# Optimization experiments

Hardware: AMD Instinct MI355X
Metric: run time of the kernel (lower is better)

The kernel has to match this reference:

```python
import jax, jax.numpy as jnp
import numpy as np

B, T, C, H = 32, 576, 1024, 16
D = C // H  # head_dim = 64

def setup_inputs() -> dict:
    key = jax.random.key(0)
    ks = jax.random.split(key, 5)
    s = 1.0 / np.sqrt(C)
    return {
        "emb_img": jax.random.normal(ks[0], (B, T, C), dtype=jnp.float32),
        "w_qkv": jax.random.normal(ks[1], (C, 3 * C), dtype=jnp.float32) * s,
        "b_qkv": jnp.zeros((3 * C,), dtype=jnp.float32),
        "w_proj": jax.random.normal(ks[2], (C, C), dtype=jnp.float32) * s,
        "b_proj": jnp.zeros((C,), dtype=jnp.float32),
    }

def reference(emb_img, w_qkv, b_qkv, w_proj, b_proj):
    # fused QKV projection
    qkv = emb_img @ w_qkv + b_qkv                       # [B,T,3C]
    q, k, v = jnp.split(qkv, 3, axis=-1)                # each [B,T,C]
    def heads(x):
        return x.reshape(B, T, H, D).transpose(0, 2, 1, 3)  # [B,H,T,D]
    q, k, v = heads(q), heads(k), heads(v)
    # note: original scales by 1/head_dim (not 1/sqrt(head_dim))
    scores = jnp.einsum("bhqd,bhkd->bhqk", q, k) * (1.0 / D)
    causal = jnp.tril(jnp.ones((T, T), dtype=bool))
    scores = jnp.where(causal[None, None], scores, -jnp.inf)
    att = jax.nn.softmax(scores, axis=-1)               # [B,H,T,T]
    y = jnp.einsum("bhqk,bhkd->bhqd", att, v)           # [B,H,T,D]
    y = y.transpose(0, 2, 1, 3).reshape(B, T, C)
    return y @ w_proj + b_proj
```

## Files before the change

kernel.cpp:

```cpp
#include <hip/hip_runtime.h>
#include <stdint.h>

namespace {

constexpr int kB = 32, kT = 576, kC = 1024, kH = 16, kD = 64;
constexpr int kM = kB * kT;
constexpr int kNqkv = 3 * kC;
constexpr float kQScale = 1.4426950408889634f / 64.0f;

typedef uint16_t u16;
typedef __attribute__((ext_vector_type(4))) float f32x4;
typedef __attribute__((ext_vector_type(8))) short short8;
typedef __attribute__((ext_vector_type(8))) __bf16 bf16x8;
typedef __attribute__((ext_vector_type(4))) uint16_t u16x4;

#define VMCNT(n) asm volatile("s_waitcnt vmcnt(" #n ")" ::: "memory")

__device__ __forceinline__ float fexp2(float x) {
  return __builtin_amdgcn_exp2f(x);
}

__device__ __forceinline__ f32x4 mfma_bf16(short8 a, short8 b, f32x4 c) {
  return __builtin_amdgcn_mfma_f32_16x16x32_bf16(
      __builtin_bit_cast(bf16x8, a), __builtin_bit_cast(bf16x8, b), c, 0, 0, 0);
}

__device__ __forceinline__ u16 to_bf16(float x) {
  uint32_t u = __float_as_uint(x);
  u += 0x7fffu + ((u >> 16) & 1u);
  return (u16)(u >> 16);
}

__device__ __forceinline__ void gload_lds16(const void* g, void* l) {
  __builtin_amdgcn_global_load_lds(
      (const __attribute__((address_space(1))) uint32_t*)(uintptr_t)g,
      (__attribute__((address_space(3))) uint32_t*)(uintptr_t)l,
      16, 0, 0);
}

__device__ __forceinline__ void bar() {
  asm volatile("" ::: "memory");
  __builtin_amdgcn_s_barrier();
  asm volatile("" ::: "memory");
}

__global__ __launch_bounds__(256) void cvt_bf16_kernel(
    const float* __restrict__ in, u16* __restrict__ out, int n4) {
  const int i = blockIdx.x * 256 + threadIdx.x;
  if (i >= n4) return;
  const f32x4 v = ((const f32x4*)in)[i];
  u16x4 o;
#pragma unroll
  for (int j = 0; j < 4; ++j) o[j] = to_bf16(v[j]);
  ((u16x4*)out)[i] = o;
}

__global__ void tconv_kernel(const float* __restrict__ in, u16* __restrict__ out,
                             int K, int N) {
  __shared__ u16 tile[32][33];
  const int nb = blockIdx.x * 32;
  const int kb = blockIdx.y * 32;
  const int tx = threadIdx.x;
  const int ty = threadIdx.y;
#pragma unroll
  for (int i = 0; i < 32; i += 8)
    tile[ty + i][tx] = to_bf16(in[(size_t)(kb + ty + i) * N + nb + tx]);
  __syncthreads();
#pragma unroll
  for (int i = 0; i < 32; i += 8)
    out[(size_t)(nb + ty + i) * K + kb + tx] = tile[tx][ty + i];
}

__global__ __launch_bounds__(512, 4) void gemm_qkv(
    const u16* __restrict__ A, const u16* __restrict__ Bt,
    const float* __restrict__ bias,
    u16* __restrict__ outQ, u16* __restrict__ outK, u16* __restrict__ outVT) {
  constexpr int Kc = 1024;
  constexpr int NT = Kc / 32;
  __shared__ char lds[3][24576];

  const int tid = threadIdx.x;
  const int wave = tid >> 6;
  const int lane = tid & 63;
  const int lo = lane & 15;
  const int hi = lane >> 4;
  const int wr = wave >> 1;
  const int wc = wave & 1;

  const int lin = blockIdx.x + blockIdx.y * 24;
  const int l2 = (lin & 7) * 216 + (lin >> 3);
  const int n0 = (l2 % 24) * 128;
  const int m0 = (l2 / 24) * 256;

  const u16* srcA[2];
#pragma unroll
  for (int c = 0; c < 2; ++c) {
    const int off = c * 8192 + tid * 16;
    const int p = off >> 7;
    const int col = (off & 127) ^ ((p & 7) << 4);
    const int Ar = (col < 64) ? p : p + 128;
    const int k_ = (col & 63) >> 1;
    srcA[c] = A + (size_t)(m0 + Ar) * Kc + k_;
  }
  const u16* srcB1;
  {
    const int off = tid * 16;
    const int p = off >> 7;
    const int col = (off & 127) ^ ((p & 7) << 4);
    const int Br = (col < 64) ? p : p + 64;
    const int k_ = (col & 63) >> 1;
    srcB1 = Bt + (size_t)(n0 + Br) * Kc + k_;
  }

  auto stage = [&](int slot, int t) {
    char* base = &lds[slot][0];
    gload_lds16(srcA[0] + t * 32, base + tid * 16);
    gload_lds16(srcA[1] + t * 32, base + 8192 + tid * 16);
    gload_lds16(srcB1 + t * 32, base + 16384 + tid * 16);
  };

  f32x4 acc[4][4] = {};

  auto compute = [&](int slot) {
    const char* base = &lds[slot][0];
    const char* baseB = base + 16384;
    const int swz = (lo & 7) << 4;
    short8 af[4], bf[4];
#pragma unroll
    for (int i = 0; i < 4; ++i) {
      const int row = wr * 64 + i * 16 + lo;
      const int prow = row & 127;
      const int half = row >> 7;
      af[i] = *(const short8*)(base + prow * 128 + ((half * 64 + hi * 16) ^ swz));
    }
#pragma unroll
    for (int j = 0; j < 4; ++j) {
      const int row = wc * 64 + j * 16 + lo;
      const int prow = row & 63;
      const int half = row >> 6;
      bf[j] = *(const short8*)(baseB + prow * 128 + ((half * 64 + hi * 16) ^ swz));
    }
    __builtin_amdgcn_s_setprio(1);
#pragma unroll
    for (int i = 0; i < 4; ++i)
#pragma unroll
      for (int j = 0; j < 4; ++j)
        acc[i][j] = mfma_bf16(af[i], bf[j], acc[i][j]);
    __builtin_amdgcn_s_setprio(0);
  };

  stage(0, 0);
  stage(1, 1);
  for (int t = 0; t < NT; ++t) {
    if (t + 1 < NT) { VMCNT(3); } else { VMCNT(0); }
    bar();
    compute(t % 3);
    if (t + 2 < NT) stage((t + 2) % 3, t + 2);
  }
  bar();

  if (n0 >= 2048) {
    u16* wlds = (u16*)&lds[0][0] + wave * (32 * 66);
    uint32_t* wlds32 = (uint32_t*)wlds;
#pragma unroll
    for (int jp = 0; jp < 2; ++jp) {
#pragma unroll
      for (int jj = 0; jj < 2; ++jj) {
        const int j = jp * 2 + jj;
        const int n = n0 + wc * 64 + j * 16 + lo;
        const float bv = bias[n];
        const int dl = jj * 16 + lo;
#pragma unroll
        for (int i = 0; i < 4; ++i)
#pragma unroll
          for (int rp = 0; rp < 2; ++rp) {
            const u16 w0 = to_bf16(acc[i][j][rp * 2] + bv);
            const u16 w1 = to_bf16(acc[i][j][rp * 2 + 1] + bv);
            wlds32[dl * 33 + i * 8 + hi * 2 + rp] =
                (uint32_t)w0 | ((uint32_t)w1 << 16);
          }
      }
#pragma unroll
      for (int p = 0; p < 8; ++p) {
        const int dl32 = p * 4 + hi;
        const int n = n0 + wc * 64 + jp * 32 + dl32;
        const int c = n & 1023;
        const int hh = c >> 6;
        const int d = c & 63;
        const int m = m0 + wr * 64 + lo * 4;
        const int bb = m / kT;
        const int t = m - bb * kT;
        const u16x4 v = *(const u16x4*)&wlds[dl32 * 66 + lo * 4];
        *(u16x4*)&outVT[((size_t)(bb * kH + hh) * kD + d) * kT + t] = v;
      }
    }
  } else {
#pragma unroll
    for (int j = 0; j < 4; ++j) {
      const int n = n0 + wc * 64 + j * 16 + lo;
      const float bv = bias[n];
      const int which = n >> 10;
      const int c = n & 1023;
      const int hh = c >> 6;
      const int d = c & 63;
#pragma unroll
      for (int i = 0; i < 4; ++i) {
        const int mrow = m0 + wr * 64 + i * 16 + hi * 4;
#pragma unroll
        for (int r = 0; r < 4; ++r) {
          const int m = mrow + r;
          const int bb = m / kT;
          const int t = m - bb * kT;
          const float v = acc[i][j][r] + bv;
          if (which == 0)
            outQ[((size_t)(bb * kH + hh) * kT + t) * kD + d] = to_bf16(v * kQScale);
          else
            outK[((size_t)(bb * kH + hh) * kT + t) * kD + d] = to_bf16(v);
        }
      }
    }
  }
}

__global__ __launch_bounds__(512, 4) void gemm_proj(
    const u16* __restrict__ A, const u16* __restrict__ Bt,
    const float* __restrict__ bias, float* __restrict__ outF) {
  constexpr int Kc = 1024;
  constexpr int NT = Kc / 32;
  __shared__ char lds[3][24576];

  const int tid = threadIdx.x;
  const int wave = tid >> 6;
  const int lane = tid & 63;
  const int lo = lane & 15;
  const int hi = lane >> 4;
  const int wr = wave >> 1;
  const int wc = wave & 1;

  const int lin = blockIdx.x + blockIdx.y * 8;
  const int l2 = (lin & 7) * 72 + (lin >> 3);
  const int n0 = (l2 % 8) * 128;
  const int m0 = (l2 / 8) * 256;

  const u16* srcA[2];
#pragma unroll
  for (int c = 0; c < 2; ++c) {
    const int off = c * 8192 + tid * 16;
    const int p = off >> 7;
    const int col = (off & 127) ^ ((p & 7) << 4);
    const int Ar = (col < 64) ? p : p + 128;
    const int k_ = (col & 63) >> 1;
    srcA[c] = A + (size_t)(m0 + Ar) * Kc + k_;
  }
  const u16* srcB1;
  {
    const int off = tid * 16;
    const int p = off >> 7;
    const int col = (off & 127) ^ ((p & 7) << 4);
    const int Br = (col < 64) ? p : p + 64;
    const int k_ = (col & 63) >> 1;
    srcB1 = Bt + (size_t)(n0 + Br) * Kc + k_;
  }

  auto stage = [&](int slot, int t) {
    char* base = &lds[slot][0];
    gload_lds16(srcA[0] + t * 32, base + tid * 16);
    gload_lds16(srcA[1] + t * 32, base + 8192 + tid * 16);
    gload_lds16(srcB1 + t * 32, base + 16384 + tid * 16);
  };

  f32x4 acc[4][4] = {};

  auto compute = [&](int slot) {
    const char* base = &lds[slot][0];
    const char* baseB = base + 16384;
    const int swz = (lo & 7) << 4;
    short8 af[4], bf[4];
#pragma unroll
    for (int i = 0; i < 4; ++i) {
      const int row = wr * 64 + i * 16 + lo;
      const int prow = row & 127;
      const int half = row >> 7;
      af[i] = *(const short8*)(base + prow * 128 + ((half * 64 + hi * 16) ^ swz));
    }
#pragma unroll
    for (int j = 0; j < 4; ++j) {
      const int row = wc * 64 + j * 16 + lo;
      const int prow = row & 63;
      const int half = row >> 6;
      bf[j] = *(const short8*)(baseB + prow * 128 + ((half * 64 + hi * 16) ^ swz));
    }
    __builtin_amdgcn_s_setprio(1);
#pragma unroll
    for (int i = 0; i < 4; ++i)
#pragma unroll
      for (int j = 0; j < 4; ++j)
        acc[i][j] = mfma_bf16(af[i], bf[j], acc[i][j]);
    __builtin_amdgcn_s_setprio(0);
  };

  stage(0, 0);
  stage(1, 1);
  for (int t = 0; t < NT; ++t) {
    if (t + 1 < NT) { VMCNT(3); } else { VMCNT(0); }
    bar();
    compute(t % 3);
    if (t + 2 < NT) stage((t + 2) % 3, t + 2);
  }

#pragma unroll
  for (int j = 0; j < 4; ++j) {
    const int n = n0 + wc * 64 + j * 16 + lo;
    const float bv = bias[n];
#pragma unroll
    for (int i = 0; i < 4; ++i) {
      const int mrow = m0 + wr * 64 + i * 16 + hi * 4;
#pragma unroll
      for (int r = 0; r < 4; ++r)
        outF[(size_t)(mrow + r) * kC + n] = acc[i][j][r] + bv;
    }
  }
}

__global__ __launch_bounds__(256) void attn_kernel(
    const u16* __restrict__ Q, const u16* __restrict__ K,
    const u16* __restrict__ VT, u16* __restrict__ Y) {
  __shared__ u16 P[4][32][72];

  const int idx = blockIdx.x;
  const int qi = 4 - (idx >> 9);
  const int bh = idx & 511;
  const int wave = threadIdx.x >> 6;
  const int lane = threadIdx.x & 63;
  const int lo = lane & 15;
  const int hi = lane >> 4;
  const int q0 = qi * 128 + wave * 32;
  if (q0 >= kT) return;

  const u16* Qb = Q + (size_t)bh * kT * kD;
  const u16* Kb = K + (size_t)bh * kT * kD;
  const u16* Vb = VT + (size_t)bh * kD * kT;

  short8 qf[2][2];
#pragma unroll
  for (int h = 0; h < 2; ++h) {
    const u16* qp = Qb + (q0 + h * 16 + lo) * kD + hi * 8;
    qf[h][0] = *(const short8*)qp;
    qf[h][1] = *(const short8*)(qp + 32);
  }

  f32x4 acc[2][4] = {};
  float mrun[2] = {-3e38f, -3e38f};
  float lsum[2] = {0.f, 0.f};

  short8 kf[4][2];
#pragma unroll
  for (int kc = 0; kc < 4; ++kc) {
    const u16* kp = Kb + (kc * 16 + lo) * kD + hi * 8;
    kf[kc][0] = *(const short8*)kp;
    kf[kc][1] = *(const short8*)(kp + 32);
  }

  const int nfull = q0 >> 6;
  const bool tail4 = ((q0 >> 5) & 1) != 0;

  auto do_tile = [&](int kv, int kclim, bool masked, bool have_next,
                     bool next_wide) {
    f32x4 s[2][4];
#pragma unroll
    for (int kc = 0; kc < 4; ++kc) {
      if (kc < kclim) {
#pragma unroll
        for (int h = 0; h < 2; ++h) {
          f32x4 z = {0.f, 0.f, 0.f, 0.f};
          z = mfma_bf16(kf[kc][0], qf[h][0], z);
          z = mfma_bf16(kf[kc][1], qf[h][1], z);
          s[h][kc] = z;
        }
      }
    }
    short8 vf[4][2];
#pragma unroll
    for (int nt = 0; nt < 4; ++nt) {
      const u16* vp = Vb + (nt * 16 + lo) * kT + kv + hi * 8;
      vf[nt][0] = *(const short8*)vp;
      if (kclim == 4) vf[nt][1] = *(const short8*)(vp + 32);
    }
    if (have_next) {
#pragma unroll
      for (int kc = 0; kc < 2; ++kc) {
        const u16* kp = Kb + (kv + 64 + kc * 16 + lo) * kD + hi * 8;
        kf[kc][0] = *(const short8*)kp;
        kf[kc][1] = *(const short8*)(kp + 32);
      }
      if (next_wide) {
#pragma unroll
        for (int kc = 2; kc < 4; ++kc) {
          const u16* kp = Kb + (kv + 64 + kc * 16 + lo) * kD + hi * 8;
          kf[kc][0] = *(const short8*)kp;
          kf[kc][1] = *(const short8*)(kp + 32);
        }
      }
    }
    if (masked) {
#pragma unroll
      for (int h = 0; h < 2; ++h) {
        const int q = q0 + h * 16 + lo;
#pragma unroll
        for (int kc = 0; kc < 4; ++kc)
          if (kc < kclim) {
#pragma unroll
            for (int r = 0; r < 4; ++r)
              if (kv + kc * 16 + hi * 4 + r > q) s[h][kc][r] = -3e38f;
          }
      }
    }
#pragma unroll
    for (int h = 0; h < 2; ++h) {
      float pm;
      {
        float m01 = fmaxf(fmaxf(s[h][0][0], s[h][0][1]),
                          fmaxf(s[h][0][2], s[h][0][3]));
        float m23 = fmaxf(fmaxf(s[h][1][0], s[h][1][1]),
                          fmaxf(s[h][1][2], s[h][1][3]));
        pm = fmaxf(m01, m23);
        if (kclim == 4) {
          float m45 = fmaxf(fmaxf(s[h][2][0], s[h][2][1]),
                            fmaxf(s[h][2][2], s[h][2][3]));
          float m67 = fmaxf(fmaxf(s[h][3][0], s[h][3][1]),
                            fmaxf(s[h][3][2], s[h][3][3]));
          pm = fmaxf(pm, fmaxf(m45, m67));
        }
      }
      pm = fmaxf(pm, __shfl_xor(pm, 16));
      pm = fmaxf(pm, __shfl_xor(pm, 32));
      const float mnew = fmaxf(mrun[h], pm);
      const float corr = fexp2(mrun[h] - mnew);
      mrun[h] = mnew;
      float psum = 0.f;
#pragma unroll
      for (int kc = 0; kc < 4; ++kc)
        if (kc < kclim) {
          u16x4 pk;
#pragma unroll
          for (int r = 0; r < 4; ++r) {
            const float pv = fexp2(s[h][kc][r] - mnew);
            psum += pv;
            pk[r] = to_bf16(pv);
          }
          *(u16x4*)&P[wave][h * 16 + lo][kc * 16 + hi * 4] = pk;
        }
      lsum[h] = lsum[h] * corr + psum;
#pragma unroll
      for (int nt = 0; nt < 4; ++nt)
#pragma unroll
        for (int r = 0; r < 4; ++r) acc[h][nt][r] *= corr;
      const short8 pf0 = *(const short8*)&P[wave][h * 16 + lo][hi * 8];
      short8 pf1;
      if (kclim == 4) pf1 = *(const short8*)&P[wave][h * 16 + lo][32 + hi * 8];
#pragma unroll
      for (int nt = 0; nt < 4; ++nt) {
        acc[h][nt] = mfma_bf16(pf0, vf[nt][0], acc[h][nt]);
        if (kclim == 4) acc[h][nt] = mfma_bf16(pf1, vf[nt][1], acc[h][nt]);
      }
    }
  };

  for (int it = 0; it < nfull; ++it)
    do_tile(it * 64, 4, false, true, (it + 1 < nfull) || tail4);
  if (tail4) do_tile(nfull * 64, 4, true, false, false);
  else       do_tile(nfull * 64, 2, true, false, false);

#pragma unroll
  for (int h = 0; h < 2; ++h) {
    lsum[h] += __shfl_xor(lsum[h], 16);
    lsum[h] += __shfl_xor(lsum[h], 32);
  }
  const int b = bh >> 4, hh = bh & 15;
#pragma unroll
  for (int h = 0; h < 2; ++h)
#pragma unroll
    for (int r = 0; r < 4; ++r) {
      const float linv = 1.0f / __shfl(lsum[h], hi * 4 + r);
      const int t = q0 + h * 16 + hi * 4 + r;
      const size_t base = ((size_t)(b * kT + t) * kH + hh) * kD;
#pragma unroll
      for (int nt = 0; nt < 4; ++nt)
        Y[base + nt * 16 + lo] = to_bf16(acc[h][nt][r] * linv);
    }
}

}

extern "C" void kernel_launch(void* const* d_in, const int* in_sizes, int n_in,
                              void* d_out, int out_size, void* d_ws, size_t ws_size,
                              hipStream_t stream) {
  (void)in_sizes; (void)n_in; (void)out_size; (void)ws_size;
  const float* emb   = (const float*)d_in[0];
  const float* wqkv  = (const float*)d_in[1];
  const float* bqkv  = (const float*)d_in[2];
  const float* wproj = (const float*)d_in[3];
  const float* bproj = (const float*)d_in[4];
  float* out = (float*)d_out;

  char* p = (char*)d_ws;
  u16* embb   = (u16*)p; p += (size_t)kM * kC * 2;
  u16* wqkvt  = (u16*)p; p += (size_t)kNqkv * kC * 2;
  u16* wprojt = (u16*)p; p += (size_t)kC * kC * 2;
  u16* Qh     = (u16*)p; p += (size_t)kM * kC * 2;
  u16* Kh     = (u16*)p; p += (size_t)kM * kC * 2;
  u16* VTh    = (u16*)p; p += (size_t)kM * kC * 2;
  u16* Yh     = (u16*)p; p += (size_t)kM * kC * 2;

  const int n4 = kM * kC / 4;
  cvt_bf16_kernel<<<dim3((n4 + 255) / 256), 256, 0, stream>>>(emb, embb, n4);
  tconv_kernel<<<dim3(kNqkv / 32, kC / 32), dim3(32, 8), 0, stream>>>(wqkv, wqkvt, kC, kNqkv);
  tconv_kernel<<<dim3(kC / 32, kC / 32), dim3(32, 8), 0, stream>>>(wproj, wprojt, kC, kC);
  gemm_qkv<<<dim3(kNqkv / 128, kM / 256), 512, 0, stream>>>(
      embb, wqkvt, bqkv, Qh, Kh, VTh);
  attn_kernel<<<dim3(5 * kB * kH), 256, 0, stream>>>(Qh, Kh, VTh, Yh);
  gemm_proj<<<dim3(kC / 128, kM / 256), 512, 0, stream>>>(
      Yh, wprojt, bproj, out);
}
```

Before: 320.2 us.

## Shrink proj GEMM tile to 128x128 with double-buffered LDS pipeline

The output-projection GEMM moves from 256x128 tiles with 512 threads and a triple-buffered LDS pipeline to 128x128 tiles with 256 threads and double buffering. This doubles the grid to 1152 blocks and cuts LDS per block, with the aim of better occupancy and CU load balance. The cost is lower operand reuse per tile and an extra barrier per k-step, since the next stage is now issued before compute. The L2-friendly block remap is adjusted to the new grid shape.

```diff
diff --git a/kernel.cpp b/kernel.cpp
--- a/kernel.cpp
+++ b/kernel.cpp
@@ -222,12 +222,12 @@
   }
 }
 
-__global__ __launch_bounds__(512, 4) void gemm_proj(
+__global__ __launch_bounds__(256, 5) void gemm_proj(
     const u16* __restrict__ A, const u16* __restrict__ Bt,
     const float* __restrict__ bias, float* __restrict__ outF) {
   constexpr int Kc = 1024;
   constexpr int NT = Kc / 32;
-  __shared__ char lds[3][24576];
+  __shared__ char lds[2][16384];
 
   const int tid = threadIdx.x;
   const int wave = tid >> 6;
@@ -238,49 +238,44 @@
   const int wc = wave & 1;
 
   const int lin = blockIdx.x + blockIdx.y * 8;
-  const int l2 = (lin & 7) * 72 + (lin >> 3);
+  const int l2 = (lin & 7) * 144 + (lin >> 3);
   const int n0 = (l2 % 8) * 128;
-  const int m0 = (l2 / 8) * 256;
+  const int m0 = (l2 / 8) * 128;
 
   const u16* srcA[2];
+  const u16* srcB[2];
 #pragma unroll
   for (int c = 0; c < 2; ++c) {
-    const int off = c * 8192 + tid * 16;
+    const int off = c * 4096 + tid * 16;
     const int p = off >> 7;
     const int col = (off & 127) ^ ((p & 7) << 4);
-    const int Ar = (col < 64) ? p : p + 128;
+    const int r_ = (col < 64) ? p : p + 64;
     const int k_ = (col & 63) >> 1;
-    srcA[c] = A + (size_t)(m0 + Ar) * Kc + k_;
-  }
-  const u16* srcB1;
-  {
-    const int off = tid * 16;
-    const int p = off >> 7;
-    const int col = (off & 127) ^ ((p & 7) << 4);
-    const int Br = (col < 64) ? p : p + 64;
-    const int k_ = (col & 63) >> 1;
-    srcB1 = Bt + (size_t)(n0 + Br) * Kc + k_;
+    srcA[c] = A + (size_t)(m0 + r_) * Kc + k_;
+    srcB[c] = Bt + (size_t)(n0 + r_) * Kc + k_;
   }
 
   auto stage = [&](int slot, int t) {
     char* base = &lds[slot][0];
-    gload_lds16(srcA[0] + t * 32, base + tid * 16);
-    gload_lds16(srcA[1] + t * 32, base + 8192 + tid * 16);
-    gload_lds16(srcB1 + t * 32, base + 16384 + tid * 16);
+#pragma unroll
+    for (int c = 0; c < 2; ++c) {
+      gload_lds16(srcA[c] + t * 32, base + c * 4096 + tid * 16);
+      gload_lds16(srcB[c] + t * 32, base + 8192 + c * 4096 + tid * 16);
+    }
   };
 
   f32x4 acc[4][4] = {};
 
   auto compute = [&](int slot) {
     const char* base = &lds[slot][0];
-    const char* baseB = base + 16384;
+    const char* baseB = base + 8192;
     const int swz = (lo & 7) << 4;
     short8 af[4], bf[4];
 #pragma unroll
     for (int i = 0; i < 4; ++i) {
       const int row = wr * 64 + i * 16 + lo;
-      const int prow = row & 127;
-      const int half = row >> 7;
+      const int prow = row & 63;
+      const int half = row >> 6;
       af[i] = *(const short8*)(base + prow * 128 + ((half * 64 + hi * 16) ^ swz));
     }
 #pragma unroll
@@ -300,12 +295,16 @@
   };
 
   stage(0, 0);
-  stage(1, 1);
   for (int t = 0; t < NT; ++t) {
-    if (t + 1 < NT) { VMCNT(3); } else { VMCNT(0); }
+    if (t + 1 < NT) {
+      stage((t + 1) & 1, t + 1);
+      VMCNT(4);
+    } else {
+      VMCNT(0);
+    }
     bar();
-    compute(t % 3);
-    if (t + 2 < NT) stage((t + 2) % 3, t + 2);
+    compute(t & 1);
+    bar();
   }
 
 #pragma unroll
@@ -519,6 +518,6 @@
   gemm_qkv<<<dim3(kNqkv / 128, kM / 256), 512, 0, stream>>>(
       embb, wqkvt, bqkv, Qh, Kh, VTh);
   attn_kernel<<<dim3(5 * kB * kH), 256, 0, stream>>>(Qh, Kh, VTh, Yh);
-  gemm_proj<<<dim3(kC / 128, kM / 256), 512, 0, stream>>>(
+  gemm_proj<<<dim3(8, kM / 128), 256, 0, stream>>>(
       Yh, wprojt, bproj, out);
 }
```

Measured after the change: 402.7 us. 1.26x slower.
